# Optimization experiments

Hardware: AMD Instinct MI355X
Metric: run time of the kernel (lower is better)

## Reference

```python
import jax, jax.numpy as jnp
import numpy as np

T, B, H = 1024, 64, 512  # seq_len, batch, hidden == input_size
MOG_STEPS = 5
N_LAYERS = 2


def setup_inputs() -> dict:
    key = jax.random.key(0)
    ks = jax.random.split(key, 8)
    s = 1.0 / np.sqrt(H)
    inp = {
        "input_seq": jax.random.normal(ks[0], (T, B, H), dtype=jnp.float32),
        # mogrifier linears: with input_size == hidden_size all are [H, H]
        "mogW": jax.random.uniform(ks[1], (N_LAYERS, MOG_STEPS, H, H), minval=-s, maxval=s, dtype=jnp.float32),
        "mogb": jax.random.uniform(ks[2], (N_LAYERS, MOG_STEPS, H), minval=-s, maxval=s, dtype=jnp.float32),
        # LSTMCell params (torch layout: W_ih [4H, I], W_hh [4H, H])
        "W_ih": jax.random.uniform(ks[3], (N_LAYERS, 4 * H, H), minval=-s, maxval=s, dtype=jnp.float32),
        "W_hh": jax.random.uniform(ks[4], (N_LAYERS, 4 * H, H), minval=-s, maxval=s, dtype=jnp.float32),
        "b_ih": jax.random.uniform(ks[5], (N_LAYERS, 4 * H), minval=-s, maxval=s, dtype=jnp.float32),
        "b_hh": jax.random.uniform(ks[6], (N_LAYERS, 4 * H), minval=-s, maxval=s, dtype=jnp.float32),
    }
    return inp


def _cell(mogW, mogb, Wih, Whh, bih, bhh, x, h, c):
    # mogrify: alternate updates, starting with x (i=0 -> x, i=1 -> h, ...)
    for i in range(MOG_STEPS):
        if (i + 1) % 2 == 0:
            h = 2.0 * jax.nn.sigmoid(x @ mogW[i].T + mogb[i]) * h
        else:
            x = 2.0 * jax.nn.sigmoid(h @ mogW[i].T + mogb[i]) * x
    # standard LSTMCell (torch gate order: i, f, g, o)
    gates = x @ Wih.T + bih + h @ Whh.T + bhh
    i_g, f_g, g_g, o_g = jnp.split(gates, 4, axis=-1)
    c_new = jax.nn.sigmoid(f_g) * c + jax.nn.sigmoid(i_g) * jnp.tanh(g_g)
    h_new = jax.nn.sigmoid(o_g) * jnp.tanh(c_new)
    return h_new, c_new


def reference(input_seq, mogW, mogb, W_ih, W_hh, b_ih, b_hh):
    B_ = input_seq.shape[1]
    z = jnp.zeros((B_, H), dtype=input_seq.dtype)

    def step(carry, x):
        h1, c1, h2, c2 = carry
        h1, c1 = _cell(mogW[0], mogb[0], W_ih[0], W_hh[0], b_ih[0], b_hh[0], x, h1, c1)
        h2, c2 = _cell(mogW[1], mogb[1], W_ih[1], W_hh[1], b_ih[1], b_hh[1], h1, h2, c2)
        return (h1, c1, h2, c2), h2

    (h1, c1, h2, c2), outputs = jax.lax.scan(step, (z, z, z, z), input_seq)
    last_hidden = jnp.stack([h1, h2], axis=0)
    last_cell = jnp.stack([c1, c2], axis=0)
    return outputs, (last_hidden, last_cell)
```

## Files before the change

kernel.cpp:

```cpp
#include <hip/hip_runtime.h>


#define T_LEN 1024
#define BB 64
#define HH 512
#define NG 4
#define GWG 64
#define NWG (NG * GWG)
#define RPG 16
#define SPIN_CAP 2000000

typedef __attribute__((ext_vector_type(8))) _Float16 f16x8;
typedef __attribute__((ext_vector_type(4))) float f32x4;

#define MW_N (2 * 5 * 512 * 512)
#define GW_N (2 * 2048 * 512)
#define ACT_N (2 * 64 * 512)

__device__ _Float16 g_mw_hi[MW_N];
__device__ _Float16 g_mw_lo[MW_N];
__device__ _Float16 g_wih_hi[GW_N];
__device__ _Float16 g_wih_lo[GW_N];
__device__ _Float16 g_whh_hi[GW_N];
__device__ _Float16 g_whh_lo[GW_N];
__device__ _Float16 g_xb_hi[ACT_N], g_xb_lo[ACT_N];
__device__ _Float16 g_hm_hi[ACT_N], g_hm_lo[ACT_N];
__device__ _Float16 g_hs_hi[ACT_N], g_hs_lo[ACT_N];
__device__ int g_slots[NWG * 32];
__device__ int g_bcast[NG * 32];

__device__ __forceinline__ float sigmoidf_(float z) {
    return 1.f / (1.f + expf(-z));
}
__device__ __forceinline__ float tanhf_(float z) {
    float a = fabsf(z);
    float e = expf(-2.f * a);
    float t = (1.f - e) / (1.f + e);
    return z >= 0.f ? t : -t;
}
__device__ __forceinline__ void split_store(_Float16* hi, _Float16* lo, int idx, float v) {
    _Float16 h = (_Float16)v;
    hi[idx] = h;
    lo[idx] = (_Float16)(v - (float)h);
}

__global__ void prep_kernel(const float* __restrict__ mogW,
                            const float* __restrict__ Wih,
                            const float* __restrict__ Whh) {
    size_t tid = (size_t)blockIdx.x * blockDim.x + threadIdx.x;
    size_t gs = (size_t)gridDim.x * blockDim.x;
    for (size_t i = tid; i < MW_N; i += gs) {
        float w = mogW[i];
        _Float16 h = (_Float16)w;
        g_mw_hi[i] = h;
        g_mw_lo[i] = (_Float16)(w - (float)h);
    }
    for (size_t i = tid; i < GW_N; i += gs) {
        float w = Wih[i];
        _Float16 h = (_Float16)w;
        g_wih_hi[i] = h;
        g_wih_lo[i] = (_Float16)(w - (float)h);
        w = Whh[i];
        h = (_Float16)w;
        g_whh_hi[i] = h;
        g_whh_lo[i] = (_Float16)(w - (float)h);
    }
    for (size_t i = tid; i < ACT_N; i += gs) {
        g_xb_hi[i] = (_Float16)0.f; g_xb_lo[i] = (_Float16)0.f;
        g_hm_hi[i] = (_Float16)0.f; g_hm_lo[i] = (_Float16)0.f;
        g_hs_hi[i] = (_Float16)0.f; g_hs_lo[i] = (_Float16)0.f;
    }
    for (size_t i = tid; i < NWG * 32; i += gs) g_slots[i] = 0;
    for (size_t i = tid; i < NG * 32; i += gs) g_bcast[i] = 0;
}

__device__ __forceinline__ void gbarrier(int g, int u6, bool master, int phase, bool* dead) {
    const int lane = threadIdx.x;
    if (lane == 0) {
        __hip_atomic_store(&g_slots[(g * GWG + u6) * 32], phase,
                           __ATOMIC_RELEASE, __HIP_MEMORY_SCOPE_AGENT);
    }
    if (*dead) return;
    if (master) {
        int* p = &g_slots[(g * GWG + lane) * 32];
        int guard = 0;
        while (__hip_atomic_load(p, __ATOMIC_RELAXED, __HIP_MEMORY_SCOPE_AGENT) < phase) {
            if (++guard > SPIN_CAP) { *dead = true; break; }
            __builtin_amdgcn_s_sleep(2);
        }
        if (lane == 0) {
            __hip_atomic_store(&g_bcast[g * 32], phase,
                               __ATOMIC_RELEASE, __HIP_MEMORY_SCOPE_AGENT);
        }
    }
    {
        int* p = &g_bcast[g * 32];
        int guard = 0;
        while (__hip_atomic_load(p, __ATOMIC_RELAXED, __HIP_MEMORY_SCOPE_AGENT) < phase) {
            if (++guard > SPIN_CAP) { *dead = true; break; }
            __builtin_amdgcn_s_sleep(2);
        }
        __builtin_amdgcn_fence(__ATOMIC_ACQUIRE, "agent");
    }
}

__device__ __forceinline__ f32x4 mm16(const _Float16* a_hi, const _Float16* a_lo,
                                      const _Float16* b_hi, const _Float16* b_lo) {
    f32x4 e = {0.f, 0.f, 0.f, 0.f};
    f32x4 o = {0.f, 0.f, 0.f, 0.f};
#pragma unroll
    for (int kb = 0; kb < 16; kb += 2) {
        f16x8 ah0 = *(const f16x8*)(a_hi + kb * 32);
        f16x8 al0 = *(const f16x8*)(a_lo + kb * 32);
        f16x8 bh0 = *(const f16x8*)(b_hi + kb * 32);
        f16x8 bl0 = *(const f16x8*)(b_lo + kb * 32);
        e = __builtin_amdgcn_mfma_f32_16x16x32_f16(ah0, bh0, e, 0, 0, 0);
        e = __builtin_amdgcn_mfma_f32_16x16x32_f16(ah0, bl0, e, 0, 0, 0);
        e = __builtin_amdgcn_mfma_f32_16x16x32_f16(al0, bh0, e, 0, 0, 0);
        f16x8 ah1 = *(const f16x8*)(a_hi + (kb + 1) * 32);
        f16x8 al1 = *(const f16x8*)(a_lo + (kb + 1) * 32);
        f16x8 bh1 = *(const f16x8*)(b_hi + (kb + 1) * 32);
        f16x8 bl1 = *(const f16x8*)(b_lo + (kb + 1) * 32);
        o = __builtin_amdgcn_mfma_f32_16x16x32_f16(ah1, bh1, o, 0, 0, 0);
        o = __builtin_amdgcn_mfma_f32_16x16x32_f16(ah1, bl1, o, 0, 0, 0);
        o = __builtin_amdgcn_mfma_f32_16x16x32_f16(al1, bh1, o, 0, 0, 0);
    }
    return e + o;
}

__global__ __launch_bounds__(64) void moglstm_kernel(
    const float* __restrict__ input_seq,
    const float* __restrict__ mogb,
    const float* __restrict__ b_ih,
    const float* __restrict__ b_hh,
    float* __restrict__ out)
{
    const int wg = blockIdx.x;
    const int g = wg >> 6;
    const int u6 = wg & 63;
    const int l = u6 >> 5;
    const int c = u6 & 31;
    const bool master = (u6 == 0);
    const int lane = threadIdx.x;
    const int al = lane & 15;
    const int ah = lane >> 4;
    const int r0 = g * RPG;

    const int mcol = c * 16 + al;
    const size_t aoff = (size_t)(r0 + al) * HH + ah * 8;
    const int lb = l * BB * HH;

    _Float16* xbh = g_xb_hi + lb; _Float16* xbl = g_xb_lo + lb;
    _Float16* hmh = g_hm_hi + lb; _Float16* hml = g_hm_lo + lb;
    _Float16* hsh = g_hs_hi + lb; _Float16* hsl = g_hs_lo + lb;

    float mbias[5];
#pragma unroll
    for (int m = 0; m < 5; ++m) mbias[m] = mogb[(l * 5 + m) * HH + mcol];
    const int jc = c * 16 + al;
    const float bgi = b_ih[l*4*HH + 0*HH + jc] + b_hh[l*4*HH + 0*HH + jc];
    const float bgf = b_ih[l*4*HH + 1*HH + jc] + b_hh[l*4*HH + 1*HH + jc];
    const float bgg = b_ih[l*4*HH + 2*HH + jc] + b_hh[l*4*HH + 2*HH + jc];
    const float bgo = b_ih[l*4*HH + 3*HH + jc] + b_hh[l*4*HH + 3*HH + jc];

    const size_t wrow = (size_t)(c * 16 + al) * HH + ah * 8;
    const _Float16* mwh[5]; const _Float16* mwl[5];
#pragma unroll
    for (int m = 0; m < 5; ++m) {
        size_t base = (size_t)(l * 5 + m) * HH * HH;
        mwh[m] = g_mw_hi + base + wrow;
        mwl[m] = g_mw_lo + base + wrow;
    }
    const _Float16* gih[4]; const _Float16* gil[4];
    const _Float16* ghh[4]; const _Float16* ghl[4];
#pragma unroll
    for (int gi = 0; gi < 4; ++gi) {
        size_t base = ((size_t)l * 4 * HH + gi * HH) * HH + wrow;
        gih[gi] = g_wih_hi + base; gil[gi] = g_wih_lo + base;
        ghh[gi] = g_whh_hi + base; ghl[gi] = g_whh_lo + base;
    }

    float c_reg[4] = {0.f, 0.f, 0.f, 0.f};
    bool dead = false;
    int phase = 0;

    for (int s = 0; s <= T_LEN; ++s) {
        const int t = (l == 0) ? s : s - 1;
        const bool active = (t >= 0) && (t < T_LEN);

        for (int m = 0; m < 5; ++m) {
            if (active) {
                const _Float16 *mvh, *mvl;
                const _Float16 *ueh, *uel;
                _Float16 *dh, *dl;
                switch (m) {
                    case 0:  mvh = hsh; mvl = hsl; ueh = nullptr; uel = nullptr; dh = xbh; dl = xbl; break;
                    case 1:  mvh = xbh; mvl = xbl; ueh = hsh; uel = hsl; dh = hmh; dl = hml; break;
                    case 2:  mvh = hmh; mvl = hml; ueh = xbh; uel = xbl; dh = xbh; dl = xbl; break;
                    case 3:  mvh = xbh; mvl = xbl; ueh = hmh; uel = hml; dh = hmh; dl = hml; break;
                    default: mvh = hmh; mvl = hml; ueh = xbh; uel = xbl; dh = xbh; dl = xbl; break;
                }
                f32x4 acc = mm16(mvh + aoff, mvl + aoff, mwh[m], mwl[m]);
#pragma unroll
                for (int r = 0; r < 4; ++r) {
                    int row = r0 + ah * 4 + r;
                    int idx = row * HH + mcol;
                    float z = acc[r] + mbias[m];
                    float sg = 2.f * sigmoidf_(z);
                    float u;
                    if (m == 0) {
                        if (l == 0)
                            u = input_seq[(size_t)t * BB * HH + idx];
                        else
                            u = (float)g_hs_hi[idx] + (float)g_hs_lo[idx];
                    } else {
                        u = (float)ueh[idx] + (float)uel[idx];
                    }
                    split_store(dh, dl, idx, sg * u);
                }
            }
            gbarrier(g, u6, master, ++phase, &dead);
        }

        if (active) {
            f32x4 acc[4];
#pragma unroll
            for (int gi = 0; gi < 4; ++gi) acc[gi] = (f32x4){0.f, 0.f, 0.f, 0.f};

            const _Float16* axh = xbh + aoff;  const _Float16* axl = xbl + aoff;
            const _Float16* amh = hmh + aoff;  const _Float16* aml = hml + aoff;
#pragma unroll
            for (int kb = 0; kb < 16; ++kb) {
                f16x8 xh = *(const f16x8*)(axh + kb * 32);
                f16x8 xl = *(const f16x8*)(axl + kb * 32);
#pragma unroll
                for (int gi = 0; gi < 4; ++gi) {
                    f16x8 bh = *(const f16x8*)(gih[gi] + kb * 32);
                    f16x8 bl = *(const f16x8*)(gil[gi] + kb * 32);
                    acc[gi] = __builtin_amdgcn_mfma_f32_16x16x32_f16(xh, bh, acc[gi], 0, 0, 0);
                    acc[gi] = __builtin_amdgcn_mfma_f32_16x16x32_f16(xh, bl, acc[gi], 0, 0, 0);
                    acc[gi] = __builtin_amdgcn_mfma_f32_16x16x32_f16(xl, bh, acc[gi], 0, 0, 0);
                }
            }
#pragma unroll
            for (int kb = 0; kb < 16; ++kb) {
                f16x8 xh = *(const f16x8*)(amh + kb * 32);
                f16x8 xl = *(const f16x8*)(aml + kb * 32);
#pragma unroll
                for (int gi = 0; gi < 4; ++gi) {
                    f16x8 bh = *(const f16x8*)(ghh[gi] + kb * 32);
                    f16x8 bl = *(const f16x8*)(ghl[gi] + kb * 32);
                    acc[gi] = __builtin_amdgcn_mfma_f32_16x16x32_f16(xh, bh, acc[gi], 0, 0, 0);
                    acc[gi] = __builtin_amdgcn_mfma_f32_16x16x32_f16(xh, bl, acc[gi], 0, 0, 0);
                    acc[gi] = __builtin_amdgcn_mfma_f32_16x16x32_f16(xl, bh, acc[gi], 0, 0, 0);
                }
            }
#pragma unroll
            for (int r = 0; r < 4; ++r) {
                int row = r0 + ah * 4 + r;
                int idx = row * HH + jc;
                float ig = sigmoidf_(acc[0][r] + bgi);
                float fg = sigmoidf_(acc[1][r] + bgf);
                float gg = tanhf_(acc[2][r] + bgg);
                float og = sigmoidf_(acc[3][r] + bgo);
                float cc = fg * c_reg[r] + ig * gg;
                c_reg[r] = cc;
                float h = og * tanhf_(cc);
                split_store(hsh, hsl, idx, h);
                if (l == 1)
                    out[(size_t)t * BB * HH + idx] = h;
                if (t == T_LEN - 1) {
                    out[(size_t)T_LEN * BB * HH + (size_t)l * BB * HH + idx] = h;
                    out[(size_t)T_LEN * BB * HH + 2u * BB * HH + (size_t)l * BB * HH + idx] = cc;
                }
            }
        }
        gbarrier(g, u6, master, ++phase, &dead);
    }
}

extern "C" void kernel_launch(void* const* d_in, const int* in_sizes, int n_in,
                              void* d_out, int out_size, void* d_ws, size_t ws_size,
                              hipStream_t stream) {
    const float* input_seq = (const float*)d_in[0];
    const float* mogW = (const float*)d_in[1];
    const float* mogb = (const float*)d_in[2];
    const float* W_ih = (const float*)d_in[3];
    const float* W_hh = (const float*)d_in[4];
    const float* b_ih = (const float*)d_in[5];
    const float* b_hh = (const float*)d_in[6];
    float* out = (float*)d_out;
    (void)d_ws; (void)ws_size;

    hipLaunchKernelGGL(prep_kernel, dim3(1024), dim3(256), 0, stream,
                       mogW, W_ih, W_hh);
    hipLaunchKernelGGL(moglstm_kernel, dim3(NWG), dim3(64), 0, stream,
                       input_seq, mogb, b_ih, b_hh, out);
}
```

Before: 120.6 ms.

## Replace two-level group barrier with flat all-lane poll and coherent loads

The master-plus-broadcast group barrier becomes a flat barrier: every workgroup polls all 64 peer slots with one lane each and combines them with a wave-wide __all, dropping the extra broadcast hop. Release/acquire fences are replaced by cache-bypassing (sc0 sc1) inline-asm loads and stores for the shared activation buffers, plus explicit vmcnt waits. Activations are batch-loaded into registers before the MFMA chains, and the elementwise operands (h, x, m) are kept in registers instead of being reloaded from global memory. Correctness now rests on the hand-written coherence scheme rather than formal memory ordering, and the spin cap was lowered.

Result: slower. 133.5 ms (+10.7%).

```diff
diff --git a/kernel.cpp b/kernel.cpp
--- a/kernel.cpp
+++ b/kernel.cpp
@@ -8,7 +8,8 @@
 #define GWG 64
 #define NWG (NG * GWG)
 #define RPG 16
-#define SPIN_CAP 2000000
+#define PAD 32
+#define SPIN_CAP 500000
 
 typedef __attribute__((ext_vector_type(8))) _Float16 f16x8;
 typedef __attribute__((ext_vector_type(4))) float f32x4;
@@ -23,11 +24,10 @@
 __device__ _Float16 g_wih_lo[GW_N];
 __device__ _Float16 g_whh_hi[GW_N];
 __device__ _Float16 g_whh_lo[GW_N];
-__device__ _Float16 g_xb_hi[ACT_N], g_xb_lo[ACT_N];
-__device__ _Float16 g_hm_hi[ACT_N], g_hm_lo[ACT_N];
-__device__ _Float16 g_hs_hi[ACT_N], g_hs_lo[ACT_N];
-__device__ int g_slots[NWG * 32];
-__device__ int g_bcast[NG * 32];
+__device__ __align__(16) _Float16 g_xh[ACT_N], g_xl[ACT_N];
+__device__ __align__(16) _Float16 g_mh[ACT_N], g_ml[ACT_N];
+__device__ __align__(16) _Float16 g_hh[ACT_N], g_hl[ACT_N];
+__device__ int g_slots[NWG * PAD];
 
 __device__ __forceinline__ float sigmoidf_(float z) {
     return 1.f / (1.f + expf(-z));
@@ -38,10 +38,29 @@
     float t = (1.f - e) / (1.f + e);
     return z >= 0.f ? t : -t;
 }
-__device__ __forceinline__ void split_store(_Float16* hi, _Float16* lo, int idx, float v) {
+
+__device__ __forceinline__ f16x8 ld_cp(const _Float16* p) {
+    f16x8 r;
+    asm volatile("global_load_dwordx4 %0, %1, off sc0 sc1" : "=v"(r) : "v"(p));
+    return r;
+}
+__device__ __forceinline__ unsigned ld_cp_u16(const _Float16* p) {
+    unsigned r;
+    asm volatile("global_load_ushort %0, %1, off sc0 sc1" : "=v"(r) : "v"(p));
+    return r;
+}
+__device__ __forceinline__ void st_cp_u16(_Float16* p, _Float16 v) {
+    asm volatile("global_store_short %0, %1, off sc0 sc1" :: "v"(p), "v"(v) : "memory");
+}
+__device__ __forceinline__ void wait_vm0() {
+    asm volatile("s_waitcnt vmcnt(0)" ::: "memory");
+    __builtin_amdgcn_sched_barrier(0);
+}
+__device__ __forceinline__ void st_hl(_Float16* ph, _Float16* pl, float v) {
     _Float16 h = (_Float16)v;
-    hi[idx] = h;
-    lo[idx] = (_Float16)(v - (float)h);
+    _Float16 l2 = (_Float16)(v - (float)h);
+    st_cp_u16(ph, h);
+    st_cp_u16(pl, l2);
 }
 
 __global__ void prep_kernel(const float* __restrict__ mogW,
@@ -66,69 +85,48 @@
         g_whh_lo[i] = (_Float16)(w - (float)h);
     }
     for (size_t i = tid; i < ACT_N; i += gs) {
-        g_xb_hi[i] = (_Float16)0.f; g_xb_lo[i] = (_Float16)0.f;
-        g_hm_hi[i] = (_Float16)0.f; g_hm_lo[i] = (_Float16)0.f;
-        g_hs_hi[i] = (_Float16)0.f; g_hs_lo[i] = (_Float16)0.f;
-    }
-    for (size_t i = tid; i < NWG * 32; i += gs) g_slots[i] = 0;
-    for (size_t i = tid; i < NG * 32; i += gs) g_bcast[i] = 0;
-}
-
-__device__ __forceinline__ void gbarrier(int g, int u6, bool master, int phase, bool* dead) {
-    const int lane = threadIdx.x;
-    if (lane == 0) {
-        __hip_atomic_store(&g_slots[(g * GWG + u6) * 32], phase,
-                           __ATOMIC_RELEASE, __HIP_MEMORY_SCOPE_AGENT);
-    }
+        g_xh[i] = (_Float16)0.f; g_xl[i] = (_Float16)0.f;
+        g_mh[i] = (_Float16)0.f; g_ml[i] = (_Float16)0.f;
+        g_hh[i] = (_Float16)0.f; g_hl[i] = (_Float16)0.f;
+    }
+    for (size_t i = tid; i < NWG * PAD; i += gs) g_slots[i] = 0;
+}
+
+__device__ __forceinline__ void gbar(int slotbase, int myslot, int phase, bool* dead) {
+    if (threadIdx.x == 0)
+        __hip_atomic_store(&g_slots[(slotbase + myslot) * PAD], phase,
+                           __ATOMIC_RELAXED, __HIP_MEMORY_SCOPE_AGENT);
     if (*dead) return;
-    if (master) {
-        int* p = &g_slots[(g * GWG + lane) * 32];
-        int guard = 0;
-        while (__hip_atomic_load(p, __ATOMIC_RELAXED, __HIP_MEMORY_SCOPE_AGENT) < phase) {
-            if (++guard > SPIN_CAP) { *dead = true; break; }
-            __builtin_amdgcn_s_sleep(2);
-        }
-        if (lane == 0) {
-            __hip_atomic_store(&g_bcast[g * 32], phase,
-                               __ATOMIC_RELEASE, __HIP_MEMORY_SCOPE_AGENT);
-        }
-    }
-    {
-        int* p = &g_bcast[g * 32];
-        int guard = 0;
-        while (__hip_atomic_load(p, __ATOMIC_RELAXED, __HIP_MEMORY_SCOPE_AGENT) < phase) {
-            if (++guard > SPIN_CAP) { *dead = true; break; }
-            __builtin_amdgcn_s_sleep(2);
-        }
-        __builtin_amdgcn_fence(__ATOMIC_ACQUIRE, "agent");
-    }
-}
-
-__device__ __forceinline__ f32x4 mm16(const _Float16* a_hi, const _Float16* a_lo,
-                                      const _Float16* b_hi, const _Float16* b_lo) {
-    f32x4 e = {0.f, 0.f, 0.f, 0.f};
-    f32x4 o = {0.f, 0.f, 0.f, 0.f};
-#pragma unroll
-    for (int kb = 0; kb < 16; kb += 2) {
-        f16x8 ah0 = *(const f16x8*)(a_hi + kb * 32);
-        f16x8 al0 = *(const f16x8*)(a_lo + kb * 32);
-        f16x8 bh0 = *(const f16x8*)(b_hi + kb * 32);
-        f16x8 bl0 = *(const f16x8*)(b_lo + kb * 32);
-        e = __builtin_amdgcn_mfma_f32_16x16x32_f16(ah0, bh0, e, 0, 0, 0);
-        e = __builtin_amdgcn_mfma_f32_16x16x32_f16(ah0, bl0, e, 0, 0, 0);
-        e = __builtin_amdgcn_mfma_f32_16x16x32_f16(al0, bh0, e, 0, 0, 0);
-        f16x8 ah1 = *(const f16x8*)(a_hi + (kb + 1) * 32);
-        f16x8 al1 = *(const f16x8*)(a_lo + (kb + 1) * 32);
-        f16x8 bh1 = *(const f16x8*)(b_hi + (kb + 1) * 32);
-        f16x8 bl1 = *(const f16x8*)(b_lo + (kb + 1) * 32);
-        o = __builtin_amdgcn_mfma_f32_16x16x32_f16(ah1, bh1, o, 0, 0, 0);
-        o = __builtin_amdgcn_mfma_f32_16x16x32_f16(ah1, bl1, o, 0, 0, 0);
-        o = __builtin_amdgcn_mfma_f32_16x16x32_f16(al1, bh1, o, 0, 0, 0);
-    }
-    return e + o;
-}
-
-__global__ __launch_bounds__(64) void moglstm_kernel(
+    int* p = &g_slots[(slotbase + (int)threadIdx.x) * PAD];
+    int guard = 0;
+    while (!__all(__hip_atomic_load(p, __ATOMIC_RELAXED, __HIP_MEMORY_SCOPE_AGENT) >= phase)) {
+        if (++guard > SPIN_CAP) { *dead = true; return; }
+        __builtin_amdgcn_s_sleep(1);
+    }
+}
+
+__device__ __forceinline__ f32x4 mogmm(const _Float16* sh, const _Float16* sl,
+                                       const _Float16* bh_, const _Float16* bl_) {
+    f16x8 Ah[16], Al[16];
+#pragma unroll
+    for (int kb = 0; kb < 16; ++kb) {
+        Ah[kb] = ld_cp(sh + kb * 32);
+        Al[kb] = ld_cp(sl + kb * 32);
+    }
+    wait_vm0();
+    f32x4 acc = {0.f, 0.f, 0.f, 0.f};
+#pragma unroll
+    for (int kb = 0; kb < 16; ++kb) {
+        f16x8 bh = *(const f16x8*)(bh_ + kb * 32);
+        f16x8 bl = *(const f16x8*)(bl_ + kb * 32);
+        acc = __builtin_amdgcn_mfma_f32_16x16x32_f16(Ah[kb], bh, acc, 0, 0, 0);
+        acc = __builtin_amdgcn_mfma_f32_16x16x32_f16(Ah[kb], bl, acc, 0, 0, 0);
+        acc = __builtin_amdgcn_mfma_f32_16x16x32_f16(Al[kb], bh, acc, 0, 0, 0);
+    }
+    return acc;
+}
+
+__global__ __launch_bounds__(64, 1) void moglstm_kernel(
     const float* __restrict__ input_seq,
     const float* __restrict__ mogb,
     const float* __restrict__ b_ih,
@@ -140,143 +138,175 @@
     const int u6 = wg & 63;
     const int l = u6 >> 5;
     const int c = u6 & 31;
-    const bool master = (u6 == 0);
     const int lane = threadIdx.x;
     const int al = lane & 15;
     const int ah = lane >> 4;
     const int r0 = g * RPG;
-
-    const int mcol = c * 16 + al;
+    const int col = c * 16 + al;
+    const int slotbase = g * GWG;
+
     const size_t aoff = (size_t)(r0 + al) * HH + ah * 8;
     const int lb = l * BB * HH;
 
-    _Float16* xbh = g_xb_hi + lb; _Float16* xbl = g_xb_lo + lb;
-    _Float16* hmh = g_hm_hi + lb; _Float16* hml = g_hm_lo + lb;
-    _Float16* hsh = g_hs_hi + lb; _Float16* hsl = g_hs_lo + lb;
+    _Float16* xh = g_xh + lb; _Float16* xl = g_xl + lb;
+    _Float16* mh = g_mh + lb; _Float16* ml = g_ml + lb;
+    _Float16* hh = g_hh + lb; _Float16* hl = g_hl + lb;
+
+    int orow[4];
+#pragma unroll
+    for (int r = 0; r < 4; ++r) orow[r] = (r0 + ah * 4 + r) * HH + col;
 
     float mbias[5];
 #pragma unroll
-    for (int m = 0; m < 5; ++m) mbias[m] = mogb[(l * 5 + m) * HH + mcol];
-    const int jc = c * 16 + al;
-    const float bgi = b_ih[l*4*HH + 0*HH + jc] + b_hh[l*4*HH + 0*HH + jc];
-    const float bgf = b_ih[l*4*HH + 1*HH + jc] + b_hh[l*4*HH + 1*HH + jc];
-    const float bgg = b_ih[l*4*HH + 2*HH + jc] + b_hh[l*4*HH + 2*HH + jc];
-    const float bgo = b_ih[l*4*HH + 3*HH + jc] + b_hh[l*4*HH + 3*HH + jc];
-
-    const size_t wrow = (size_t)(c * 16 + al) * HH + ah * 8;
-    const _Float16* mwh[5]; const _Float16* mwl[5];
-#pragma unroll
-    for (int m = 0; m < 5; ++m) {
-        size_t base = (size_t)(l * 5 + m) * HH * HH;
-        mwh[m] = g_mw_hi + base + wrow;
-        mwl[m] = g_mw_lo + base + wrow;
-    }
-    const _Float16* gih[4]; const _Float16* gil[4];
-    const _Float16* ghh[4]; const _Float16* ghl[4];
-#pragma unroll
-    for (int gi = 0; gi < 4; ++gi) {
-        size_t base = ((size_t)l * 4 * HH + gi * HH) * HH + wrow;
-        gih[gi] = g_wih_hi + base; gil[gi] = g_wih_lo + base;
-        ghh[gi] = g_whh_hi + base; ghl[gi] = g_whh_lo + base;
-    }
+    for (int m = 0; m < 5; ++m) mbias[m] = mogb[(l * 5 + m) * HH + col];
+    const float bgi = b_ih[l*4*HH + 0*HH + col] + b_hh[l*4*HH + 0*HH + col];
+    const float bgf = b_ih[l*4*HH + 1*HH + col] + b_hh[l*4*HH + 1*HH + col];
+    const float bgg = b_ih[l*4*HH + 2*HH + col] + b_hh[l*4*HH + 2*HH + col];
+    const float bgo = b_ih[l*4*HH + 3*HH + col] + b_hh[l*4*HH + 3*HH + col];
+
+    const size_t wrow = (size_t)col * HH + ah * 8;
+    const _Float16* mwhB = g_mw_hi + (size_t)l * 5 * HH * HH + wrow;
+    const _Float16* mwlB = g_mw_lo + (size_t)l * 5 * HH * HH + wrow;
+    const _Float16* wihH = g_wih_hi + (size_t)l * 4 * HH * HH + wrow;
+    const _Float16* wihL = g_wih_lo + (size_t)l * 4 * HH * HH + wrow;
+    const _Float16* whhH = g_whh_hi + (size_t)l * 4 * HH * HH + wrow;
+    const _Float16* whhL = g_whh_lo + (size_t)l * 4 * HH * HH + wrow;
 
     float c_reg[4] = {0.f, 0.f, 0.f, 0.f};
+    float hreg[4] = {0.f, 0.f, 0.f, 0.f};
+    float xreg[4], mreg[4];
     bool dead = false;
     int phase = 0;
+
+#define MOG_STAGE(mI, SH, SL, DH, DL, UE_EXPR)                                \
+    {                                                                         \
+        f32x4 acc = mogmm(SH + aoff, SL + aoff,                               \
+                          mwhB + (size_t)(mI) * HH * HH,                      \
+                          mwlB + (size_t)(mI) * HH * HH);                     \
+        _Pragma("unroll")                                                     \
+        for (int r = 0; r < 4; ++r) {                                         \
+            float z = acc[r] + mbias[mI];                                     \
+            float nv = 2.f * sigmoidf_(z) * (UE_EXPR);                        \
+            if ((mI) & 1) mreg[r] = nv; else xreg[r] = nv;                    \
+            st_hl(DH + orow[r], DL + orow[r], nv);                            \
+        }                                                                     \
+        wait_vm0();                                                           \
+    }
 
     for (int s = 0; s <= T_LEN; ++s) {
         const int t = (l == 0) ? s : s - 1;
         const bool active = (t >= 0) && (t < T_LEN);
 
-        for (int m = 0; m < 5; ++m) {
-            if (active) {
-                const _Float16 *mvh, *mvl;
-                const _Float16 *ueh, *uel;
-                _Float16 *dh, *dl;
-                switch (m) {
-                    case 0:  mvh = hsh; mvl = hsl; ueh = nullptr; uel = nullptr; dh = xbh; dl = xbl; break;
-                    case 1:  mvh = xbh; mvl = xbl; ueh = hsh; uel = hsl; dh = hmh; dl = hml; break;
-                    case 2:  mvh = hmh; mvl = hml; ueh = xbh; uel = xbl; dh = xbh; dl = xbl; break;
-                    case 3:  mvh = xbh; mvl = xbl; ueh = hmh; uel = hml; dh = hmh; dl = hml; break;
-                    default: mvh = hmh; mvl = hml; ueh = xbh; uel = xbl; dh = xbh; dl = xbl; break;
-                }
-                f32x4 acc = mm16(mvh + aoff, mvl + aoff, mwh[m], mwl[m]);
+        if (active) {
+            float u_in[4];
+            if (l == 0) {
+#pragma unroll
+                for (int r = 0; r < 4; ++r)
+                    u_in[r] = input_seq[(size_t)t * BB * HH + orow[r]];
+                MOG_STAGE(0, hh, hl, xh, xl, u_in[r]);
+            } else {
+                unsigned uhb[4], ulb[4];
 #pragma unroll
                 for (int r = 0; r < 4; ++r) {
-                    int row = r0 + ah * 4 + r;
-                    int idx = row * HH + mcol;
-                    float z = acc[r] + mbias[m];
-                    float sg = 2.f * sigmoidf_(z);
-                    float u;
-                    if (m == 0) {
-                        if (l == 0)
-                            u = input_seq[(size_t)t * BB * HH + idx];
-                        else
-                            u = (float)g_hs_hi[idx] + (float)g_hs_lo[idx];
-                    } else {
-                        u = (float)ueh[idx] + (float)uel[idx];
+                    uhb[r] = ld_cp_u16(g_hh + orow[r]);
+                    ulb[r] = ld_cp_u16(g_hl + orow[r]);
+                }
+                f32x4 acc = mogmm(hh + aoff, hl + aoff, mwhB, mwlB);
+#pragma unroll
+                for (int r = 0; r < 4; ++r) {
+                    float uv = (float)__builtin_bit_cast(_Float16, (unsigned short)uhb[r])
+                             + (float)__builtin_bit_cast(_Float16, (unsigned short)ulb[r]);
+                    u_in[r] = uv;
+                    float z = acc[r] + mbias[0];
+                    float nv = 2.f * sigmoidf_(z) * uv;
+                    xreg[r] = nv;
+                    st_hl(xh + orow[r], xl + orow[r], nv);
+                }
+                wait_vm0();
+            }
+        }
+        gbar(slotbase, u6, ++phase, &dead);
+
+        if (active) MOG_STAGE(1, xh, xl, mh, ml, hreg[r]);
+        gbar(slotbase, u6, ++phase, &dead);
+
+        if (active) MOG_STAGE(2, mh, ml, xh, xl, xreg[r]);
+        gbar(slotbase, u6, ++phase, &dead);
+
+        if (active) MOG_STAGE(3, xh, xl, mh, ml, mreg[r]);
+        gbar(slotbase, u6, ++phase, &dead);
+
+        if (active) MOG_STAGE(4, mh, ml, xh, xl, xreg[r]);
+        gbar(slotbase, u6, ++phase, &dead);
+
+        if (active) {
+            f32x4 a0 = {0.f,0.f,0.f,0.f}, a1 = {0.f,0.f,0.f,0.f};
+            f32x4 a2 = {0.f,0.f,0.f,0.f}, a3 = {0.f,0.f,0.f,0.f};
+            {
+                f16x8 Ah[16], Al[16];
+#pragma unroll
+                for (int kb = 0; kb < 16; ++kb) {
+                    Ah[kb] = ld_cp(xh + aoff + kb * 32);
+                    Al[kb] = ld_cp(xl + aoff + kb * 32);
+                }
+                wait_vm0();
+#pragma unroll
+                for (int kb = 0; kb < 16; ++kb) {
+#pragma unroll
+                    for (int gi = 0; gi < 4; ++gi) {
+                        f16x8 bh = *(const f16x8*)(wihH + (size_t)gi * HH * HH + kb * 32);
+                        f16x8 bl = *(const f16x8*)(wihL + (size_t)gi * HH * HH + kb * 32);
+                        f32x4* A = gi == 0 ? &a0 : gi == 1 ? &a1 : gi == 2 ? &a2 : &a3;
+                        *A = __builtin_amdgcn_mfma_f32_16x16x32_f16(Ah[kb], bh, *A, 0, 0, 0);
+                        *A = __builtin_amdgcn_mfma_f32_16x16x32_f16(Ah[kb], bl, *A, 0, 0, 0);
+                        *A = __builtin_amdgcn_mfma_f32_16x16x32_f16(Al[kb], bh, *A, 0, 0, 0);
                     }
-                    split_store(dh, dl, idx, sg * u);
                 }
             }
-            gbarrier(g, u6, master, ++phase, &dead);
-        }
-
-        if (active) {
-            f32x4 acc[4];
-#pragma unroll
-            for (int gi = 0; gi < 4; ++gi) acc[gi] = (f32x4){0.f, 0.f, 0.f, 0.f};
-
-            const _Float16* axh = xbh + aoff;  const _Float16* axl = xbl + aoff;
-            const _Float16* amh = hmh + aoff;  const _Float16* aml = hml + aoff;
-#pragma unroll
-            for (int kb = 0; kb < 16; ++kb) {
-                f16x8 xh = *(const f16x8*)(axh + kb * 32);
-                f16x8 xl = *(const f16x8*)(axl + kb * 32);
-#pragma unroll
-                for (int gi = 0; gi < 4; ++gi) {
-                    f16x8 bh = *(const f16x8*)(gih[gi] + kb * 32);
-                    f16x8 bl = *(const f16x8*)(gil[gi] + kb * 32);
-                    acc[gi] = __builtin_amdgcn_mfma_f32_16x16x32_f16(xh, bh, acc[gi], 0, 0, 0);
-                    acc[gi] = __builtin_amdgcn_mfma_f32_16x16x32_f16(xh, bl, acc[gi], 0, 0, 0);
-                    acc[gi] = __builtin_amdgcn_mfma_f32_16x16x32_f16(xl, bh, acc[gi], 0, 0, 0);
+            {
+                f16x8 Ah[16], Al[16];
+#pragma unroll
+                for (int kb = 0; kb < 16; ++kb) {
+                    Ah[kb] = ld_cp(mh + aoff + kb * 32);
+                    Al[kb] = ld_cp(ml + aoff + kb * 32);
+                }
+                wait_vm0();
+#pragma unroll
+                for (int kb = 0; kb < 16; ++kb) {
+#pragma unroll
+                    for (int gi = 0; gi < 4; ++gi) {
+                        f16x8 bh = *(const f16x8*)(whhH + (size_t)gi * HH * HH + kb * 32);
+                        f16x8 bl = *(const f16x8*)(whhL + (size_t)gi * HH * HH + kb * 32);
+                        f32x4* A = gi == 0 ? &a0 : gi == 1 ? &a1 : gi == 2 ? &a2 : &a3;
+                        *A = __builtin_amdgcn_mfma_f32_16x16x32_f16(Ah[kb], bh, *A, 0, 0, 0);
+                        *A = __builtin_amdgcn_mfma_f32_16x16x32_f16(Ah[kb], bl, *A, 0, 0, 0);
+                        *A = __builtin_amdgcn_mfma_f32_16x16x32_f16(Al[kb], bh, *A, 0, 0, 0);
+                    }
                 }
             }
 #pragma unroll
-            for (int kb = 0; kb < 16; ++kb) {
-                f16x8 xh = *(const f16x8*)(amh + kb * 32);
-                f16x8 xl = *(const f16x8*)(aml + kb * 32);
-#pragma unroll
-                for (int gi = 0; gi < 4; ++gi) {
-                    f16x8 bh = *(const f16x8*)(ghh[gi] + kb * 32);
-                    f16x8 bl = *(const f16x8*)(ghl[gi] + kb * 32);
-                    acc[gi] = __builtin_amdgcn_mfma_f32_16x16x32_f16(xh, bh, acc[gi], 0, 0, 0);
-                    acc[gi] = __builtin_amdgcn_mfma_f32_16x16x32_f16(xh, bl, acc[gi], 0, 0, 0);
-                    acc[gi] = __builtin_amdgcn_mfma_f32_16x16x32_f16(xl, bh, acc[gi], 0, 0, 0);
-                }
-            }
-#pragma unroll
             for (int r = 0; r < 4; ++r) {
-                int row = r0 + ah * 4 + r;
-                int idx = row * HH + jc;
-                float ig = sigmoidf_(acc[0][r] + bgi);
-                float fg = sigmoidf_(acc[1][r] + bgf);
-                float gg = tanhf_(acc[2][r] + bgg);
-                float og = sigmoidf_(acc[3][r] + bgo);
+                float ig = sigmoidf_(a0[r] + bgi);
+                float fg = sigmoidf_(a1[r] + bgf);
+                float gg = tanhf_(a2[r] + bgg);
+                float og = sigmoidf_(a3[r] + bgo);
                 float cc = fg * c_reg[r] + ig * gg;
                 c_reg[r] = cc;
                 float h = og * tanhf_(cc);
-                split_store(hsh, hsl, idx, h);
+                hreg[r] = h;
+                st_hl(hh + orow[r], hl + orow[r], h);
                 if (l == 1)
-                    out[(size_t)t * BB * HH + idx] = h;
+                    out[(size_t)t * BB * HH + orow[r]] = h;
                 if (t == T_LEN - 1) {
-                    out[(size_t)T_LEN * BB * HH + (size_t)l * BB * HH + idx] = h;
-                    out[(size_t)T_LEN * BB * HH + 2u * BB * HH + (size_t)l * BB * HH + idx] = cc;
+                    out[(size_t)T_LEN * BB * HH + (size_t)l * BB * HH + orow[r]] = h;
+                    out[(size_t)T_LEN * BB * HH + 2u * BB * HH + (size_t)l * BB * HH + orow[r]] = cc;
                 }
             }
+            wait_vm0();
         }
-        gbarrier(g, u6, master, ++phase, &dead);
-    }
+        gbar(slotbase, u6, ++phase, &dead);
+    }
+#undef MOG_STAGE
 }
 
 extern "C" void kernel_launch(void* const* d_in, const int* in_sizes, int n_in,
```
